# Optimization experiments

Measured on AMD Instinct MI355X. Metric: run time of the kernel, lower is better.

The kernel has to match this reference:

```python
import jax, jax.numpy as jnp
import numpy as np

BETA = 0.25
EPS = 1e-10


def setup_inputs() -> dict:
    key = jax.random.key(0)
    k1, k2 = jax.random.split(key)
    z = jax.random.normal(k1, (16, 256, 32, 32), dtype=jnp.float32)
    # Original init: uniform(-1/n_embed, 1/n_embed)
    n_embed, embed_dim = 8192, 256
    codebook = jax.random.uniform(k2, (n_embed, embed_dim), dtype=jnp.float32,
                                  minval=-1.0 / n_embed, maxval=1.0 / n_embed)
    return {"z": z, "codebook": codebook}


def reference(z, codebook):
    B, C, H, W = z.shape
    n_embed = codebook.shape[0]
    zp = jnp.transpose(z, (0, 2, 3, 1))            # (B,H,W,C)
    zf = zp.reshape(-1, C)                          # (N,C)
    # squared L2 distances (N, n_embed)
    d = (jnp.sum(zf * zf, axis=1, keepdims=True)
         + jnp.sum(codebook * codebook, axis=1)
         - 2.0 * zf @ codebook.T)
    idx = jnp.argmin(d, axis=1)                     # (N,)
    zq = codebook[idx].reshape(zp.shape)            # gather == one-hot @ codebook
    commitment_loss = jnp.mean((jax.lax.stop_gradient(zq) - zp) ** 2)
    embedding_loss = jnp.mean((zq - jax.lax.stop_gradient(zp)) ** 2)
    loss = embedding_loss + BETA * commitment_loss
    # straight-through estimator
    zq_st = zp + jax.lax.stop_gradient(zq - zp)
    # perplexity from mean one-hot usage (counts / N)
    counts = jnp.zeros((n_embed,), dtype=zf.dtype).at[idx].add(1.0)
    avg_probs = counts / zf.shape[0]
    perplexity = jnp.exp(-jnp.sum(avg_probs * jnp.log(avg_probs + EPS)))
    zq_out = jnp.transpose(zq_st, (0, 3, 1, 2))     # (B,C,H,W)
    return zq_out, loss, perplexity, idx
```

## Files before the change

### kernel.cpp

```cpp
#include <hip/hip_runtime.h>
#include <math.h>

#define Nrows 16384
#define NE 8192
#define Kdim 256
#define HWsz 1024
#define NSPL 4
#define BETAF 0.25f
#define NGATHBLK 1024

typedef __attribute__((ext_vector_type(8))) short bf16x8;
typedef __attribute__((ext_vector_type(16))) float f32x16;
typedef unsigned short u16;

__device__ inline u16 bf16_rne(float x) {
  unsigned int u = __float_as_uint(x);
  return (u16)((u + 0x7FFFu + ((u >> 16) & 1u)) >> 16);
}
__device__ inline float bf16_tof(u16 h) {
  return __uint_as_float(((unsigned int)h) << 16);
}
__device__ inline void gll16(const void* g, void* l) {
  __builtin_amdgcn_global_load_lds(
      (const __attribute__((address_space(1))) unsigned int*)g,
      (__attribute__((address_space(3))) unsigned int*)l, 16, 0, 0);
}

__global__ __launch_bounds__(256) void cc_kernel(const float* __restrict__ cb,
                                                 float* __restrict__ cc) {
  int wave = threadIdx.x >> 6;
  int lane = threadIdx.x & 63;
  int row = blockIdx.x * 4 + wave;
  const float4 v = *(const float4*)(cb + (size_t)row * Kdim + lane * 4);
  float s = v.x * v.x + v.y * v.y + v.z * v.z + v.w * v.w;
  for (int off = 32; off; off >>= 1) s += __shfl_down(s, off);
  if (lane == 0) cc[row] = s;
}

__global__ __launch_bounds__(256) void conv_cb(const float* __restrict__ cb,
                                               u16* __restrict__ Cf) {
  const int g = blockIdx.x * 256 + threadIdx.x;
  const int j = g >> 4, k16 = g & 15;
  const float* src = cb + (size_t)j * Kdim + k16 * 16;
  float f[16];
#pragma unroll
  for (int q = 0; q < 4; ++q) {
    const float4 v = ((const float4*)src)[q];
    f[q * 4 + 0] = v.x; f[q * 4 + 1] = v.y; f[q * 4 + 2] = v.z; f[q * 4 + 3] = v.w;
  }
  u16 h[3][16];
#pragma unroll
  for (int i = 0; i < 16; ++i) {
    const u16 q0 = bf16_rne(f[i]);
    const float r1 = f[i] - bf16_tof(q0);
    const u16 q1 = bf16_rne(r1);
    const float r2 = r1 - bf16_tof(q1);
    h[0][i] = q0; h[1][i] = q1; h[2][i] = bf16_rne(r2);
  }
  const int j32 = j >> 5, li = j & 31;
#pragma unroll
  for (int arr = 0; arr < 3; ++arr) {
#pragma unroll
    for (int kh = 0; kh < 2; ++kh) {
      const size_t off = ((size_t)(j32 * 3 + arr) * 16 + k16) * 512 + (kh * 32 + li) * 8;
      *(int4*)(Cf + off) = *(int4*)&h[arr][kh * 8];
    }
  }
}

__global__ __launch_bounds__(256) void conv_z(const float* __restrict__ z,
                                              u16* __restrict__ Zf,
                                              float* __restrict__ zz) {
  __shared__ float tile[64][68];
  const int t = threadIdx.x;
  const int bid = blockIdx.x;
  const int n0 = bid * 64;
  const int b = bid >> 4;
  const int hw0 = (bid & 15) << 6;
  const float* zb = z + (size_t)b * (Kdim * HWsz) + hw0;
  float zzacc = 0.f;
  const int rr = t >> 2;
  const int kq = (t & 3) * 16;
  for (int kc = 0; kc < 4; ++kc) {
#pragma unroll
    for (int i = 0; i < 16; ++i) {
      const int idx = i * 256 + t;
      const int k = idx >> 6, r = idx & 63;
      tile[r][k] = zb[(size_t)(kc * 64 + k) * HWsz + r];
    }
    __syncthreads();
    if (t < 64) {
      for (int k = 0; k < 64; ++k) {
        const float a = tile[t][k];
        zzacc = fmaf(a, a, zzacc);
      }
    }
    u16 h[3][16];
#pragma unroll
    for (int i = 0; i < 16; ++i) {
      const float fv = tile[rr][kq + i];
      const u16 q0 = bf16_rne(fv);
      const float r1 = fv - bf16_tof(q0);
      const u16 q1 = bf16_rne(r1);
      const float r2 = r1 - bf16_tof(q1);
      h[0][i] = q0; h[1][i] = q1; h[2][i] = bf16_rne(r2);
    }
    const int k16 = kc * 4 + (t & 3);
    const int n32 = bid * 2 + (rr >> 5), li = rr & 31;
#pragma unroll
    for (int arr = 0; arr < 3; ++arr) {
#pragma unroll
      for (int kh = 0; kh < 2; ++kh) {
        const size_t off = ((size_t)(n32 * 3 + arr) * 16 + k16) * 512 + (kh * 32 + li) * 8;
        *(int4*)(Zf + off) = *(int4*)&h[arr][kh * 8];
      }
    }
    __syncthreads();
  }
  if (t < 64) zz[n0 + t] = zzacc;
}

__global__ __launch_bounds__(256, 2) void vq_gemm(
    const u16* __restrict__ Cf, const u16* __restrict__ Zf,
    const float* __restrict__ cc, const float* __restrict__ zz,
    float* __restrict__ pd, int* __restrict__ pj) {
  __shared__ __align__(16) u16 Al[3][12288];
  __shared__ float ccs[2048];

  const int t = threadIdx.x;
  const int lane = t & 63;
  const int w = __builtin_amdgcn_readfirstlane(t >> 6);
  const int bid = blockIdx.x;
  const int cg = bid & 3;
  const int rt = bid >> 2;
  const int n32 = rt * 4 + w;

#pragma unroll
  for (int i = 0; i < 8; ++i) ccs[i * 256 + t] = cc[cg * 2048 + i * 256 + t];

  const float zzv = zz[n32 * 32 + (lane & 31)];

  bf16x8 B[16][3];
#pragma unroll
  for (int kc = 0; kc < 16; ++kc)
#pragma unroll
    for (int arr = 0; arr < 3; ++arr)
      B[kc][arr] = *(const bf16x8*)(
          Zf + ((size_t)(n32 * 3 + arr) * 16 + kc) * 512 + lane * 8);

#define STAGE(gg, c_, sl)                                                     \
  {                                                                           \
    const int ggc_ = (gg) < 32 ? (gg) : 0;                                    \
    _Pragma("unroll")                                                         \
    for (int i = 0; i < 6; ++i) {                                             \
      const int s = w * 6 + i;                                                \
      const int jx = s / 12, rem = s % 12;                                    \
      const int kc2 = rem / 3, arr = rem % 3;                                 \
      gll16(Cf + ((size_t)((cg * 64 + ggc_ * 2 + jx) * 3 + arr) * 16 +        \
                  ((c_) * 4 + kc2)) * 512 + lane * 8,                         \
            &Al[sl][((jx * 4 + kc2) * 3 + arr) * 512]);                       \
    }                                                                         \
  }

#define MF(af, bv, ac) ac = __builtin_amdgcn_mfma_f32_32x32x16_bf16(af, bv, ac, 0, 0, 0);
#define CHUNK(sl, c_)                                                         \
  _Pragma("unroll")                                                           \
  for (int kc2 = 0; kc2 < 4; ++kc2) {                                         \
    bf16x8 a0[3], a1[3];                                                      \
    _Pragma("unroll")                                                         \
    for (int arr = 0; arr < 3; ++arr) {                                       \
      a0[arr] = *(const bf16x8*)&Al[sl][(kc2 * 3 + arr) * 512 + lane * 8];    \
      a1[arr] = *(const bf16x8*)&Al[sl][((4 + kc2) * 3 + arr) * 512 + lane * 8]; \
    }                                                                         \
    MF(a0[0], B[(c_) * 4 + kc2][0], acc0) MF(a1[0], B[(c_) * 4 + kc2][0], acc1) \
    MF(a0[0], B[(c_) * 4 + kc2][1], acc0) MF(a1[0], B[(c_) * 4 + kc2][1], acc1) \
    MF(a0[1], B[(c_) * 4 + kc2][0], acc0) MF(a1[1], B[(c_) * 4 + kc2][0], acc1) \
    MF(a0[1], B[(c_) * 4 + kc2][1], acc0) MF(a1[1], B[(c_) * 4 + kc2][1], acc1) \
    MF(a0[0], B[(c_) * 4 + kc2][2], acc0) MF(a1[0], B[(c_) * 4 + kc2][2], acc1) \
    MF(a0[2], B[(c_) * 4 + kc2][0], acc0) MF(a1[2], B[(c_) * 4 + kc2][0], acc1) \
  }

#define WTB()                                                                 \
  __builtin_amdgcn_sched_barrier(0);                                          \
  asm volatile("s_waitcnt vmcnt(6)" ::: "memory");                            \
  __builtin_amdgcn_s_barrier();                                               \
  __builtin_amdgcn_sched_barrier(0);

#define ROT() { sl = (sl == 2) ? 0 : sl + 1; s2 = (s2 == 2) ? 0 : s2 + 1; }

  STAGE(0, 0, 0)
  STAGE(0, 1, 1)
  asm volatile("s_waitcnt lgkmcnt(0)" ::: "memory");
  __builtin_amdgcn_sched_barrier(0);

  float bd = INFINITY;
  int bj = 0;
  const f32x16 zero16 = {0,0,0,0,0,0,0,0,0,0,0,0,0,0,0,0};
  int sl = 0, s2 = 2;

  for (int g = 0; g < 32; ++g) {
    f32x16 acc0 = zero16, acc1 = zero16;
    WTB() STAGE(g, 2, s2)     CHUNK(sl, 0) ROT()
    WTB() STAGE(g, 3, s2)     CHUNK(sl, 1) ROT()
    WTB() STAGE(g + 1, 0, s2) CHUNK(sl, 2) ROT()
    WTB() STAGE(g + 1, 1, s2) CHUNK(sl, 3) ROT()

#pragma unroll
    for (int jx = 0; jx < 2; ++jx) {
      const f32x16& a = jx ? acc1 : acc0;
#pragma unroll
      for (int q = 0; q < 4; ++q) {
        const float4 c4 = *(const float4*)&ccs[g * 64 + jx * 32 + q * 8 + (lane >> 5) * 4];
        const float cv[4] = {c4.x, c4.y, c4.z, c4.w};
#pragma unroll
        for (int r = 0; r < 4; ++r) {
          const float d = (zzv + cv[r]) - 2.0f * a[q * 4 + r];
          const int j = cg * 2048 + g * 64 + jx * 32 + r + q * 8 + (lane >> 5) * 4;
          if (d < bd) { bd = d; bj = j; }
        }
      }
    }
  }
  asm volatile("s_waitcnt vmcnt(0)" ::: "memory");
#undef STAGE
#undef CHUNK
#undef MF
#undef WTB
#undef ROT

  {
    const float od = __shfl_xor(bd, 32);
    const int oj = __shfl_xor(bj, 32);
    if (od < bd || (od == bd && oj < bj)) { bd = od; bj = oj; }
  }
  if (lane < 32) {
    const int n = n32 * 32 + lane;
    pd[(size_t)cg * Nrows + n] = bd;
    pj[(size_t)cg * Nrows + n] = bj;
  }
}

__global__ __launch_bounds__(256) void vq_gather_loss(
    const float* __restrict__ z, const float* __restrict__ cb,
    const float* __restrict__ pd, const int* __restrict__ pj,
    float* __restrict__ outz, float* __restrict__ out_idxf,
    int* __restrict__ counts, float* __restrict__ loss_part) {
  __shared__ float cbl[64 * 65];
  __shared__ int jr[64];
  __shared__ float ws4[4];
  const int t = threadIdx.x;
  const int bid = blockIdx.x;
  const int nt = bid >> 2;
  const int cq = bid & 3;
  const int b = nt >> 4;
  const int hw0 = (nt & 15) << 6;
  const int n0 = b * HWsz + hw0;

  if (t < 64) {
    const int n = n0 + t;
    float d0 = pd[n];
    int j0 = pj[n];
    for (int s = 1; s < NSPL; ++s) {
      const float d = pd[(size_t)s * Nrows + n];
      const int j = pj[(size_t)s * Nrows + n];
      if (d < d0 || (d == d0 && j < j0)) { d0 = d; j0 = j; }
    }
    jr[t] = j0;
    if (cq == 0) {
      out_idxf[n] = (float)j0;
      atomicAdd(&counts[j0], 1);
    }
  }
  __syncthreads();

  {
    const int r = t >> 2;
    const int c0 = (t & 3) * 16;
    const int j = jr[r];
    const float* src = cb + (size_t)j * Kdim + cq * 64 + c0;
#pragma unroll
    for (int q = 0; q < 4; ++q) {
      const float4 v = ((const float4*)src)[q];
      float* dst = &cbl[r * 65 + c0 + q * 4];
      dst[0] = v.x; dst[1] = v.y; dst[2] = v.z; dst[3] = v.w;
    }
  }
  __syncthreads();

  const int w = t >> 6, lane = t & 63;

  float ls = 0.f;
  for (int k = 0; k < 16; ++k) {
    const int cl = w * 16 + k;
    const int c = cq * 64 + cl;
    const float q = cbl[lane * 65 + cl];
    const size_t gidx = ((size_t)(b * Kdim + c)) * HWsz + hw0 + lane;
    const float zv = z[gidx];
    outz[gidx] = q;
    const float dd = q - zv;
    ls = fmaf(dd, dd, ls);
  }
  for (int off = 32; off; off >>= 1) ls += __shfl_down(ls, off);
  if (lane == 0) ws4[w] = ls;
  __syncthreads();
  if (t == 0) loss_part[bid] = (ws4[0] + ws4[1]) + (ws4[2] + ws4[3]);
}

__global__ __launch_bounds__(256) void vq_final(const int* __restrict__ counts,
                                                const float* __restrict__ loss_part,
                                                float* __restrict__ out_sc) {
  float h = 0.f;
  for (int i = threadIdx.x; i < NE; i += 256) {
    float p = (float)counts[i] * (1.0f / 16384.0f);
    h += p * logf(p + 1e-10f);
  }
  float ls = 0.f;
  for (int i = threadIdx.x; i < NGATHBLK; i += 256) ls += loss_part[i];
  for (int off = 32; off; off >>= 1) {
    h += __shfl_down(h, off);
    ls += __shfl_down(ls, off);
  }
  __shared__ float hs[4], lss[4];
  if ((threadIdx.x & 63) == 0) {
    hs[threadIdx.x >> 6] = h;
    lss[threadIdx.x >> 6] = ls;
  }
  __syncthreads();
  if (threadIdx.x == 0) {
    float H = (hs[0] + hs[1]) + (hs[2] + hs[3]);
    float L = (lss[0] + lss[1]) + (lss[2] + lss[3]);
    float m = L * (1.0f / 4194304.0f);
    out_sc[0] = m + BETAF * m;
    out_sc[1] = expf(-H);
  }
}

extern "C" void kernel_launch(void* const* d_in, const int* in_sizes, int n_in,
                              void* d_out, int out_size, void* d_ws, size_t ws_size,
                              hipStream_t stream) {
  const float* z = (const float*)d_in[0];
  const float* cb = (const float*)d_in[1];
  float* out = (float*)d_out;
  float* out_zq = out;
  float* out_sc = out + 4194304;
  float* out_idx = out + 4194306;

  char* wp = (char*)d_ws;
  u16* Cf = (u16*)wp;           wp += (size_t)NE * Kdim * 2 * 3;
  u16* Zf = (u16*)wp;           wp += (size_t)Nrows * Kdim * 2 * 3;
  float* cc = (float*)wp;       wp += (size_t)NE * 4;
  float* zz = (float*)wp;       wp += (size_t)Nrows * 4;
  float* pd = (float*)wp;       wp += (size_t)NSPL * Nrows * 4;
  int* pj = (int*)wp;           wp += (size_t)NSPL * Nrows * 4;
  int* counts = (int*)wp;       wp += (size_t)NE * 4;
  float* loss_part = (float*)wp; wp += (size_t)NGATHBLK * 4;

  hipMemsetAsync(counts, 0, (size_t)NE * 4, stream);

  cc_kernel<<<NE / 4, 256, 0, stream>>>(cb, cc);
  conv_cb<<<NE * 16 / 256, 256, 0, stream>>>(cb, Cf);
  conv_z<<<Nrows / 64, 256, 0, stream>>>(z, Zf, zz);
  vq_gemm<<<512, 256, 0, stream>>>(Cf, Zf, cc, zz, pd, pj);
  vq_gather_loss<<<NGATHBLK, 256, 0, stream>>>(z, cb, pd, pj, out_zq, out_idx,
                                               counts, loss_part);
  vq_final<<<1, 256, 0, stream>>>(counts, loss_part, out_sc);
}
```

Measured before the change: 420.2 us.

## Split codebook into eight column groups with smaller pipeline stages

Doubles the codebook split of the distance GEMM from 4 to 8 groups. This doubles the grid to 1024 blocks and halves each block's share of the codebook. Each pipeline stage now loads half as much K-data, so shared memory per block shrinks and the launch bound is raised to target 4 blocks per CU. The aim is better occupancy and load balance across CUs. In exchange, every block still loads the full 48-register Z operand set, so Z traffic and register pressure at the higher occupancy target go up, and barriers become more frequent.

Measured after the change: 651.0 us. +54.9%, slower.

```diff
diff --git a/kernel.cpp b/kernel.cpp
--- a/kernel.cpp
+++ b/kernel.cpp
@@ -5,7 +5,7 @@
 #define NE 8192
 #define Kdim 256
 #define HWsz 1024
-#define NSPL 4
+#define NSPL 8
 #define BETAF 0.25f
 #define NGATHBLK 1024
 
@@ -120,23 +120,23 @@
   if (t < 64) zz[n0 + t] = zzacc;
 }
 
-__global__ __launch_bounds__(256, 2) void vq_gemm(
+__global__ __launch_bounds__(256, 4) void vq_gemm(
     const u16* __restrict__ Cf, const u16* __restrict__ Zf,
     const float* __restrict__ cc, const float* __restrict__ zz,
     float* __restrict__ pd, int* __restrict__ pj) {
-  __shared__ __align__(16) u16 Al[3][12288];
-  __shared__ float ccs[2048];
+  __shared__ __align__(16) u16 Al[3][6144];
+  __shared__ float ccs[1024];
 
   const int t = threadIdx.x;
   const int lane = t & 63;
   const int w = __builtin_amdgcn_readfirstlane(t >> 6);
   const int bid = blockIdx.x;
-  const int cg = bid & 3;
-  const int rt = bid >> 2;
+  const int cg = bid & 7;
+  const int rt = bid >> 3;
   const int n32 = rt * 4 + w;
 
 #pragma unroll
-  for (int i = 0; i < 8; ++i) ccs[i * 256 + t] = cc[cg * 2048 + i * 256 + t];
+  for (int i = 0; i < 4; ++i) ccs[i * 256 + t] = cc[cg * 1024 + i * 256 + t];
 
   const float zzv = zz[n32 * 32 + (lane & 31)];
 
@@ -148,48 +148,50 @@
       B[kc][arr] = *(const bf16x8*)(
           Zf + ((size_t)(n32 * 3 + arr) * 16 + kc) * 512 + lane * 8);
 
-#define STAGE(gg, c_, sl)                                                     \
+#define STAGE(P, sl_)                                                         \
   {                                                                           \
-    const int ggc_ = (gg) < 32 ? (gg) : 0;                                    \
+    const int gg_ = (P) >> 3;                                                 \
+    const int ggc_ = gg_ < 16 ? gg_ : 0;                                      \
+    const int hh_ = (P) & 7;                                                  \
     _Pragma("unroll")                                                         \
-    for (int i = 0; i < 6; ++i) {                                             \
-      const int s = w * 6 + i;                                                \
-      const int jx = s / 12, rem = s % 12;                                    \
-      const int kc2 = rem / 3, arr = rem % 3;                                 \
-      gll16(Cf + ((size_t)((cg * 64 + ggc_ * 2 + jx) * 3 + arr) * 16 +        \
-                  ((c_) * 4 + kc2)) * 512 + lane * 8,                         \
-            &Al[sl][((jx * 4 + kc2) * 3 + arr) * 512]);                       \
+    for (int i = 0; i < 3; ++i) {                                             \
+      const int s = w * 3 + i;                                                \
+      const int jx = s / 6, rem = s % 6;                                      \
+      const int kcl = rem / 3, arr = rem % 3;                                 \
+      gll16(Cf + ((size_t)((cg * 32 + ggc_ * 2 + jx) * 3 + arr) * 16 +        \
+                  (hh_ * 2 + kcl)) * 512 + lane * 8,                          \
+            &Al[sl_][((jx * 2 + kcl) * 3 + arr) * 512]);                      \
     }                                                                         \
   }
 
 #define MF(af, bv, ac) ac = __builtin_amdgcn_mfma_f32_32x32x16_bf16(af, bv, ac, 0, 0, 0);
-#define CHUNK(sl, c_)                                                         \
+#define CHUNK(sl_, h_)                                                        \
   _Pragma("unroll")                                                           \
-  for (int kc2 = 0; kc2 < 4; ++kc2) {                                         \
+  for (int kcl = 0; kcl < 2; ++kcl) {                                         \
     bf16x8 a0[3], a1[3];                                                      \
     _Pragma("unroll")                                                         \
     for (int arr = 0; arr < 3; ++arr) {                                       \
-      a0[arr] = *(const bf16x8*)&Al[sl][(kc2 * 3 + arr) * 512 + lane * 8];    \
-      a1[arr] = *(const bf16x8*)&Al[sl][((4 + kc2) * 3 + arr) * 512 + lane * 8]; \
+      a0[arr] = *(const bf16x8*)&Al[sl_][(kcl * 3 + arr) * 512 + lane * 8];   \
+      a1[arr] = *(const bf16x8*)&Al[sl_][((2 + kcl) * 3 + arr) * 512 + lane * 8]; \
     }                                                                         \
-    MF(a0[0], B[(c_) * 4 + kc2][0], acc0) MF(a1[0], B[(c_) * 4 + kc2][0], acc1) \
-    MF(a0[0], B[(c_) * 4 + kc2][1], acc0) MF(a1[0], B[(c_) * 4 + kc2][1], acc1) \
-    MF(a0[1], B[(c_) * 4 + kc2][0], acc0) MF(a1[1], B[(c_) * 4 + kc2][0], acc1) \
-    MF(a0[1], B[(c_) * 4 + kc2][1], acc0) MF(a1[1], B[(c_) * 4 + kc2][1], acc1) \
-    MF(a0[0], B[(c_) * 4 + kc2][2], acc0) MF(a1[0], B[(c_) * 4 + kc2][2], acc1) \
-    MF(a0[2], B[(c_) * 4 + kc2][0], acc0) MF(a1[2], B[(c_) * 4 + kc2][0], acc1) \
+    MF(a0[0], B[(h_) * 2 + kcl][0], acc0) MF(a1[0], B[(h_) * 2 + kcl][0], acc1) \
+    MF(a0[0], B[(h_) * 2 + kcl][1], acc0) MF(a1[0], B[(h_) * 2 + kcl][1], acc1) \
+    MF(a0[1], B[(h_) * 2 + kcl][0], acc0) MF(a1[1], B[(h_) * 2 + kcl][0], acc1) \
+    MF(a0[1], B[(h_) * 2 + kcl][1], acc0) MF(a1[1], B[(h_) * 2 + kcl][1], acc1) \
+    MF(a0[0], B[(h_) * 2 + kcl][2], acc0) MF(a1[0], B[(h_) * 2 + kcl][2], acc1) \
+    MF(a0[2], B[(h_) * 2 + kcl][0], acc0) MF(a1[2], B[(h_) * 2 + kcl][0], acc1) \
   }
 
 #define WTB()                                                                 \
   __builtin_amdgcn_sched_barrier(0);                                          \
-  asm volatile("s_waitcnt vmcnt(6)" ::: "memory");                            \
+  asm volatile("s_waitcnt vmcnt(3)" ::: "memory");                            \
   __builtin_amdgcn_s_barrier();                                               \
   __builtin_amdgcn_sched_barrier(0);
 
 #define ROT() { sl = (sl == 2) ? 0 : sl + 1; s2 = (s2 == 2) ? 0 : s2 + 1; }
 
-  STAGE(0, 0, 0)
-  STAGE(0, 1, 1)
+  STAGE(0, 0)
+  STAGE(1, 1)
   asm volatile("s_waitcnt lgkmcnt(0)" ::: "memory");
   __builtin_amdgcn_sched_barrier(0);
 
@@ -198,12 +200,15 @@
   const f32x16 zero16 = {0,0,0,0,0,0,0,0,0,0,0,0,0,0,0,0};
   int sl = 0, s2 = 2;
 
-  for (int g = 0; g < 32; ++g) {
+  for (int g = 0; g < 16; ++g) {
     f32x16 acc0 = zero16, acc1 = zero16;
-    WTB() STAGE(g, 2, s2)     CHUNK(sl, 0) ROT()
-    WTB() STAGE(g, 3, s2)     CHUNK(sl, 1) ROT()
-    WTB() STAGE(g + 1, 0, s2) CHUNK(sl, 2) ROT()
-    WTB() STAGE(g + 1, 1, s2) CHUNK(sl, 3) ROT()
+#pragma unroll
+    for (int h = 0; h < 8; ++h) {
+      WTB()
+      STAGE(g * 8 + h + 2, s2)
+      CHUNK(sl, h)
+      ROT()
+    }
 
 #pragma unroll
     for (int jx = 0; jx < 2; ++jx) {
@@ -215,7 +220,7 @@
 #pragma unroll
         for (int r = 0; r < 4; ++r) {
           const float d = (zzv + cv[r]) - 2.0f * a[q * 4 + r];
-          const int j = cg * 2048 + g * 64 + jx * 32 + r + q * 8 + (lane >> 5) * 4;
+          const int j = cg * 1024 + g * 64 + jx * 32 + r + q * 8 + (lane >> 5) * 4;
           if (d < bd) { bd = d; bj = j; }
         }
       }
@@ -360,7 +365,7 @@
   cc_kernel<<<NE / 4, 256, 0, stream>>>(cb, cc);
   conv_cb<<<NE * 16 / 256, 256, 0, stream>>>(cb, Cf);
   conv_z<<<Nrows / 64, 256, 0, stream>>>(z, Zf, zz);
-  vq_gemm<<<512, 256, 0, stream>>>(Cf, Zf, cc, zz, pd, pj);
+  vq_gemm<<<1024, 256, 0, stream>>>(Cf, Zf, cc, zz, pd, pj);
   vq_gather_loss<<<NGATHBLK, 256, 0, stream>>>(z, cb, pd, pj, out_zq, out_idx,
                                                counts, loss_part);
   vq_final<<<1, 256, 0, stream>>>(counts, loss_part, out_sc);
```

## Give each wave a private LDS ring to drop block barriers in GEMM loop

Applied to the files above, without the earlier changes.

The main GEMM loop previously staged shared codebook tiles cooperatively across all four waves and synchronized with a workgroup barrier every chunk. Now each wave loads its own copy of the codebook slice into a private three-slot LDS ring, one k-step at a time, and waits only on its own vmcnt, removing s_barrier from the loop. The cost is four-fold redundant global/L2 traffic for the codebook tile (each wave fetches the same data) and finer-grained, smaller pipeline stages with more loop iterations.

Measured after the change: 500.7 us. 1.19x slower.

```diff
diff --git a/kernel.cpp b/kernel.cpp
--- a/kernel.cpp
+++ b/kernel.cpp
@@ -124,7 +124,7 @@
     const u16* __restrict__ Cf, const u16* __restrict__ Zf,
     const float* __restrict__ cc, const float* __restrict__ zz,
     float* __restrict__ pd, int* __restrict__ pj) {
-  __shared__ __align__(16) u16 Al[3][12288];
+  __shared__ __align__(16) u16 Al[4][3][3072];
   __shared__ float ccs[2048];
 
   const int t = threadIdx.x;
@@ -148,50 +148,46 @@
       B[kc][arr] = *(const bf16x8*)(
           Zf + ((size_t)(n32 * 3 + arr) * 16 + kc) * 512 + lane * 8);
 
-#define STAGE(gg, c_, sl)                                                     \
+  u16* Aw = &Al[w][0][0];
+
+#define STAGE(P, SL)                                                          \
   {                                                                           \
-    const int ggc_ = (gg) < 32 ? (gg) : 0;                                    \
+    const int pp_ = (P);                                                      \
+    const int gg_ = pp_ >> 4;                                                 \
+    const int ggc_ = gg_ < 32 ? gg_ : 0;                                      \
+    const int kc_ = pp_ & 15;                                                 \
     _Pragma("unroll")                                                         \
     for (int i = 0; i < 6; ++i) {                                             \
-      const int s = w * 6 + i;                                                \
-      const int jx = s / 12, rem = s % 12;                                    \
-      const int kc2 = rem / 3, arr = rem % 3;                                 \
-      gll16(Cf + ((size_t)((cg * 64 + ggc_ * 2 + jx) * 3 + arr) * 16 +        \
-                  ((c_) * 4 + kc2)) * 512 + lane * 8,                         \
-            &Al[sl][((jx * 4 + kc2) * 3 + arr) * 512]);                       \
+      const int jx = i / 3, arr = i % 3;                                      \
+      gll16(Cf + ((size_t)((cg * 64 + ggc_ * 2 + jx) * 3 + arr) * 16 + kc_)   \
+                    * 512 + lane * 8,                                         \
+            Aw + (SL) * 3072 + i * 512);                                      \
     }                                                                         \
   }
 
 #define MF(af, bv, ac) ac = __builtin_amdgcn_mfma_f32_32x32x16_bf16(af, bv, ac, 0, 0, 0);
-#define CHUNK(sl, c_)                                                         \
-  _Pragma("unroll")                                                           \
-  for (int kc2 = 0; kc2 < 4; ++kc2) {                                         \
+#define CHUNK(kcv)                                                            \
+  {                                                                           \
+    const u16* Ab = Aw + sl * 3072;                                           \
     bf16x8 a0[3], a1[3];                                                      \
     _Pragma("unroll")                                                         \
     for (int arr = 0; arr < 3; ++arr) {                                       \
-      a0[arr] = *(const bf16x8*)&Al[sl][(kc2 * 3 + arr) * 512 + lane * 8];    \
-      a1[arr] = *(const bf16x8*)&Al[sl][((4 + kc2) * 3 + arr) * 512 + lane * 8]; \
+      a0[arr] = *(const bf16x8*)(Ab + arr * 512 + lane * 8);                  \
+      a1[arr] = *(const bf16x8*)(Ab + (3 + arr) * 512 + lane * 8);            \
     }                                                                         \
-    MF(a0[0], B[(c_) * 4 + kc2][0], acc0) MF(a1[0], B[(c_) * 4 + kc2][0], acc1) \
-    MF(a0[0], B[(c_) * 4 + kc2][1], acc0) MF(a1[0], B[(c_) * 4 + kc2][1], acc1) \
-    MF(a0[1], B[(c_) * 4 + kc2][0], acc0) MF(a1[1], B[(c_) * 4 + kc2][0], acc1) \
-    MF(a0[1], B[(c_) * 4 + kc2][1], acc0) MF(a1[1], B[(c_) * 4 + kc2][1], acc1) \
-    MF(a0[0], B[(c_) * 4 + kc2][2], acc0) MF(a1[0], B[(c_) * 4 + kc2][2], acc1) \
-    MF(a0[2], B[(c_) * 4 + kc2][0], acc0) MF(a1[2], B[(c_) * 4 + kc2][0], acc1) \
-  }
-
-#define WTB()                                                                 \
-  __builtin_amdgcn_sched_barrier(0);                                          \
-  asm volatile("s_waitcnt vmcnt(6)" ::: "memory");                            \
-  __builtin_amdgcn_s_barrier();                                               \
-  __builtin_amdgcn_sched_barrier(0);
+    MF(a0[0], B[kcv][0], acc0) MF(a1[0], B[kcv][0], acc1)                     \
+    MF(a0[0], B[kcv][1], acc0) MF(a1[0], B[kcv][1], acc1)                     \
+    MF(a0[1], B[kcv][0], acc0) MF(a1[1], B[kcv][0], acc1)                     \
+    MF(a0[1], B[kcv][1], acc0) MF(a1[1], B[kcv][1], acc1)                     \
+    MF(a0[0], B[kcv][2], acc0) MF(a1[0], B[kcv][2], acc1)                     \
+    MF(a0[2], B[kcv][0], acc0) MF(a1[2], B[kcv][0], acc1)                     \
+  }
 
 #define ROT() { sl = (sl == 2) ? 0 : sl + 1; s2 = (s2 == 2) ? 0 : s2 + 1; }
 
-  STAGE(0, 0, 0)
-  STAGE(0, 1, 1)
-  asm volatile("s_waitcnt lgkmcnt(0)" ::: "memory");
-  __builtin_amdgcn_sched_barrier(0);
+  STAGE(0, 0)
+  STAGE(1, 1)
+  __syncthreads();
 
   float bd = INFINITY;
   int bj = 0;
@@ -200,10 +196,15 @@
 
   for (int g = 0; g < 32; ++g) {
     f32x16 acc0 = zero16, acc1 = zero16;
-    WTB() STAGE(g, 2, s2)     CHUNK(sl, 0) ROT()
-    WTB() STAGE(g, 3, s2)     CHUNK(sl, 1) ROT()
-    WTB() STAGE(g + 1, 0, s2) CHUNK(sl, 2) ROT()
-    WTB() STAGE(g + 1, 1, s2) CHUNK(sl, 3) ROT()
+#pragma unroll
+    for (int kc = 0; kc < 16; ++kc) {
+      __builtin_amdgcn_sched_barrier(0);
+      STAGE(g * 16 + kc + 2, s2)
+      asm volatile("s_waitcnt vmcnt(12)" ::: "memory");
+      __builtin_amdgcn_sched_barrier(0);
+      CHUNK(kc)
+      ROT()
+    }
 
 #pragma unroll
     for (int jx = 0; jx < 2; ++jx) {
@@ -225,7 +226,6 @@
 #undef STAGE
 #undef CHUNK
 #undef MF
-#undef WTB
 #undef ROT
 
   {
```
